# Kernel tuning notes

Measured on AMD Instinct MI355X. Metric: run time of the kernel, lower is better.

The kernel has to match this reference:

```python
import jax, jax.numpy as jnp
import numpy as np

DIM = 1024
HEADS = 16
HEAD_DIM = DIM // HEADS
RANK = 4
AUDIO_DIM = 768


def _lora(x, A, B):
    # x: [..., in]; A: [rank, in]; B: [out, rank]
    return x + (x @ A.T @ B.T) * (1.0 / RANK)


def setup_inputs() -> dict:
    key = jax.random.key(0)
    ks = jax.random.split(key, 20)
    s = 0.02
    inp = {
        "x": jax.random.normal(ks[0], (1, 4096, DIM), jnp.float32),
        "audio_features": jax.random.normal(ks[1], (1, 1024, AUDIO_DIM), jnp.float32),
        "q_w": jax.random.normal(ks[2], (DIM, DIM), jnp.float32) * s,
        "q_b": jnp.zeros((DIM,), jnp.float32),
        "k_w": jax.random.normal(ks[3], (DIM, DIM), jnp.float32) * s,
        "k_b": jnp.zeros((DIM,), jnp.float32),
        "v_w": jax.random.normal(ks[4], (DIM, DIM), jnp.float32) * s,
        "v_b": jnp.zeros((DIM,), jnp.float32),
        "o_w": jax.random.normal(ks[5], (DIM, DIM), jnp.float32) * s,
        "o_b": jnp.zeros((DIM,), jnp.float32),
        "a_w": jax.random.normal(ks[6], (DIM, AUDIO_DIM), jnp.float32) * s,
        "a_b": jnp.zeros((DIM,), jnp.float32),
        "qA": jax.random.normal(ks[7], (RANK, DIM), jnp.float32) * 0.01,
        "qB": jax.random.normal(ks[8], (DIM, RANK), jnp.float32) * 0.01,
        "kA": jax.random.normal(ks[9], (RANK, DIM), jnp.float32) * 0.01,
        "kB": jax.random.normal(ks[10], (DIM, RANK), jnp.float32) * 0.01,
        "vA": jax.random.normal(ks[11], (RANK, DIM), jnp.float32) * 0.01,
        "vB": jax.random.normal(ks[12], (DIM, RANK), jnp.float32) * 0.01,
    }
    return inp


def reference(x, audio_features, q_w, q_b, k_w, k_b, v_w, v_b, o_w, o_b,
              a_w, a_b, qA, qB, kA, kB, vA, vB):
    B, N, C = x.shape
    # audio projection: Linear(768 -> dim), torch Linear is x @ W.T + b
    audio = audio_features @ a_w.T + a_b  # [B, M, C]
    M = audio.shape[1]

    q = _lora(x @ q_w.T + q_b, qA, qB)      # [B, N, C]
    k = _lora(audio @ k_w.T + k_b, kA, kB)  # [B, M, C]
    v = _lora(audio @ v_w.T + v_b, vA, vB)  # [B, M, C]

    q = q.reshape(B, N, HEADS, HEAD_DIM).transpose(0, 2, 1, 3)  # [B,H,N,d]
    k = k.reshape(B, M, HEADS, HEAD_DIM).transpose(0, 2, 1, 3)  # [B,H,M,d]
    v = v.reshape(B, M, HEADS, HEAD_DIM).transpose(0, 2, 1, 3)  # [B,H,M,d]

    scale = HEAD_DIM ** -0.5
    attn = jnp.einsum('bhnd,bhmd->bhnm', q, k) * scale  # [B,H,N,M]
    attn = jax.nn.softmax(attn, axis=-1)
    out = jnp.einsum('bhnm,bhmd->bhnd', attn, v)        # [B,H,N,d]
    out = out.transpose(0, 2, 1, 3).reshape(B, N, C)
    return out @ o_w.T + o_b
```

## Files before the change

kernel.cpp:

```cpp
#include <hip/hip_runtime.h>
#include <math.h>

#define DIM 1024
#define HEADS 16
#define HD 64
#define QSCALE 0.1803368801111204f

typedef __attribute__((ext_vector_type(8))) short short8;
typedef __attribute__((ext_vector_type(4))) float f32x4;
typedef unsigned short ushort_t;

#define MFMA(a, b, c) __builtin_amdgcn_mfma_f32_16x16x32_bf16(a, b, c, 0, 0, 0)
#define VMCNT(n) asm volatile("s_waitcnt vmcnt(" #n ")" ::: "memory")
#define BARRIER() __builtin_amdgcn_s_barrier()

__device__ __forceinline__ ushort_t f2bf(float f) {
    union { float f; unsigned u; } v; v.f = f;
    unsigned r = v.u + 0x7FFF + ((v.u >> 16) & 1);
    return (ushort_t)(r >> 16);
}
__device__ __forceinline__ void gl2lds16(const void* g, void* l) {
    __builtin_amdgcn_global_load_lds(
        (const __attribute__((address_space(1))) unsigned*)g,
        (__attribute__((address_space(3))) unsigned*)l, 16, 0, 0);
}

#define C_X  1048576
#define C_AF 196608
__global__ __launch_bounds__(256) void prep1(
    const float* __restrict__ x, const float* __restrict__ af,
    const float* __restrict__ aw, const float* __restrict__ ow,
    ushort_t* __restrict__ xb, ushort_t* __restrict__ afb,
    ushort_t* __restrict__ awb, ushort_t* __restrict__ owb,
    const float* __restrict__ qw, const float* __restrict__ kw,
    const float* __restrict__ vw,
    const float* __restrict__ qA, const float* __restrict__ kA,
    const float* __restrict__ vA,
    float* __restrict__ part)
{
    const int b = blockIdx.x, tid = threadIdx.x;
    if (b >= 48) {
        int c = (b - 48) * 256 + tid;
        const float* s; ushort_t* d; int off;
        if (c < C_X)               { s = x;  d = xb;  off = c; }
        else if (c < C_X + C_AF)   { s = af; d = afb; off = c - C_X; }
        else if (c < C_X + 2*C_AF) { s = aw; d = awb; off = c - C_X - C_AF; }
        else                       { s = ow; d = owb; off = c - C_X - 2*C_AF; }
        float4 v = ((const float4*)s)[off];
        ushort4 o = { f2bf(v.x), f2bf(v.y), f2bf(v.z), f2bf(v.w) };
        ((ushort4*)d)[off] = o;
        return;
    }
    const int pb = b;
    const int proj = pb >> 4, chunk = pb & 15;
    const float* W = proj == 0 ? qw : proj == 1 ? kw : vw;
    const float* A = proj == 0 ? qA : proj == 1 ? kA : vA;
    const float4* W4 = (const float4*)W;

    float4 acc0 = {0,0,0,0}, acc1 = {0,0,0,0}, acc2 = {0,0,0,0}, acc3 = {0,0,0,0};
    const int o0 = chunk * 64;
    for (int o = o0; o < o0 + 64; ++o) {
        float4 wrow = W4[o * 256 + tid];
        float a0 = A[o], a1 = A[1024 + o], a2 = A[2048 + o], a3 = A[3072 + o];
        acc0.x += a0 * wrow.x; acc0.y += a0 * wrow.y; acc0.z += a0 * wrow.z; acc0.w += a0 * wrow.w;
        acc1.x += a1 * wrow.x; acc1.y += a1 * wrow.y; acc1.z += a1 * wrow.z; acc1.w += a1 * wrow.w;
        acc2.x += a2 * wrow.x; acc2.y += a2 * wrow.y; acc2.z += a2 * wrow.z; acc2.w += a2 * wrow.w;
        acc3.x += a3 * wrow.x; acc3.y += a3 * wrow.y; acc3.z += a3 * wrow.z; acc3.w += a3 * wrow.w;
    }
    float4* P4 = (float4*)part;
    P4[(pb * 4 + 0) * 256 + tid] = acc0;
    P4[(pb * 4 + 1) * 256 + tid] = acc1;
    P4[(pb * 4 + 2) * 256 + tid] = acc2;
    P4[(pb * 4 + 3) * 256 + tid] = acc3;
}

__global__ __launch_bounds__(256) void prep2(
    const float* __restrict__ qw, const float* __restrict__ kw,
    const float* __restrict__ vw,
    const float* __restrict__ qA, const float* __restrict__ kA,
    const float* __restrict__ vA,
    const float* __restrict__ qB, const float* __restrict__ kB,
    const float* __restrict__ vB,
    const float* __restrict__ qb, const float* __restrict__ kb,
    const float* __restrict__ vb,
    const float* __restrict__ part,
    ushort_t* __restrict__ wqe, ushort_t* __restrict__ wke,
    ushort_t* __restrict__ wve, float* __restrict__ beff)
{
    const int b = blockIdx.x, tid = threadIdx.x;
    const int proj = b >> 4, chunk = b & 15;
    const float* W = proj == 0 ? qw : proj == 1 ? kw : vw;
    const float* A = proj == 0 ? qA : proj == 1 ? kA : vA;
    const float* B = proj == 0 ? qB : proj == 1 ? kB : vB;
    const float* bias = proj == 0 ? qb : proj == 1 ? kb : vb;
    ushort_t* Weff = proj == 0 ? wqe : proj == 1 ? wke : wve;
    const float scale = proj == 0 ? QSCALE : 1.0f;
    const float4* W4 = (const float4*)W;
    const float4* P4 = (const float4*)part;

    __shared__ float T1s[4096];
    #pragma unroll
    for (int r = 0; r < 4; ++r) {
        float4 s = {0, 0, 0, 0};
        for (int blk = 0; blk < 16; ++blk) {
            float4 p = P4[((proj * 16 + blk) * 4 + r) * 256 + tid];
            s.x += p.x; s.y += p.y; s.z += p.z; s.w += p.w;
        }
        *(float4*)(T1s + r * 1024 + tid * 4) = s;
    }
    __syncthreads();

    float4 t0 = *(const float4*)(T1s + tid * 4);
    float4 t1 = *(const float4*)(T1s + 1024 + tid * 4);
    float4 t2 = *(const float4*)(T1s + 2048 + tid * 4);
    float4 t3 = *(const float4*)(T1s + 3072 + tid * 4);

    const int o0 = chunk * 64;
    for (int o = o0; o < o0 + 64; ++o) {
        float4 wrow = W4[o * 256 + tid];
        float4 Bo = *(const float4*)(B + o * 4);
        ushort4 out;
        out.x = f2bf((wrow.x + 0.25f * (Bo.x*t0.x + Bo.y*t1.x + Bo.z*t2.x + Bo.w*t3.x)) * scale);
        out.y = f2bf((wrow.y + 0.25f * (Bo.x*t0.y + Bo.y*t1.y + Bo.z*t2.y + Bo.w*t3.y)) * scale);
        out.z = f2bf((wrow.z + 0.25f * (Bo.x*t0.z + Bo.y*t1.z + Bo.z*t2.z + Bo.w*t3.z)) * scale);
        out.w = f2bf((wrow.w + 0.25f * (Bo.x*t0.w + Bo.y*t1.w + Bo.z*t2.w + Bo.w*t3.w)) * scale);
        *(ushort4*)(Weff + (size_t)o * 1024 + tid * 4) = out;
    }

    if (chunk == 0) {
        float bt[4] = {0.f, 0.f, 0.f, 0.f};
        for (int o = tid; o < 1024; o += 256) {
            float bo = bias[o];
            bt[0] = fmaf(A[o], bo, bt[0]);
            bt[1] = fmaf(A[1024 + o], bo, bt[1]);
            bt[2] = fmaf(A[2048 + o], bo, bt[2]);
            bt[3] = fmaf(A[3072 + o], bo, bt[3]);
        }
        #pragma unroll
        for (int r = 0; r < 4; ++r)
            #pragma unroll
            for (int off = 32; off; off >>= 1) bt[r] += __shfl_xor(bt[r], off);
        __shared__ float btr[4][4];
        if ((tid & 63) == 0) {
            #pragma unroll
            for (int r = 0; r < 4; ++r) btr[r][tid >> 6] = bt[r];
        }
        __syncthreads();
        float b0 = btr[0][0] + btr[0][1] + btr[0][2] + btr[0][3];
        float b1 = btr[1][0] + btr[1][1] + btr[1][2] + btr[1][3];
        float b2 = btr[2][0] + btr[2][1] + btr[2][2] + btr[2][3];
        float b3 = btr[3][0] + btr[3][1] + btr[3][2] + btr[3][3];
        for (int o = tid; o < 1024; o += 256) {
            float4 Bo = *(const float4*)(B + o * 4);
            beff[proj * 1024 + o] =
                (bias[o] + 0.25f * (Bo.x*b0 + Bo.y*b1 + Bo.z*b2 + Bo.w*b3)) * scale;
        }
    }
}

template<int OUTF32>
__device__ __forceinline__ void gemm4_body(
    char* lds, const ushort_t* __restrict__ A, const ushort_t* __restrict__ W,
    const float* __restrict__ bias, void* __restrict__ C,
    int N, int K, int bm, int bn)
{
    const int tid = threadIdx.x, lane = tid & 63, wv = tid >> 6;
    const int l15 = lane & 15, l4 = lane >> 4;
    const int wm = wv >> 1, wn = wv & 1;

    const ushort_t *Ag[2], *Wg;
    #pragma unroll
    for (int c = 0; c < 2; ++c) {
        int f = c * 256 + tid, ra = f >> 2, ga = (f & 3) ^ ((ra >> 1) & 3);
        Ag[c] = A + (size_t)(bm * 128 + ra) * K + ga * 8;
    }
    {
        int f = tid, rb = f >> 2, gb = (f & 3) ^ ((rb >> 1) & 3);
        Wg = W + (size_t)(bn * 64 + rb) * K + gb * 8;
    }
    int aoff[4], woff[2];
    #pragma unroll
    for (int m = 0; m < 4; ++m) {
        int r = wm * 64 + m * 16 + l15;
        aoff[m] = r * 64 + ((l4 ^ ((r >> 1) & 3)) << 4);
    }
    #pragma unroll
    for (int n = 0; n < 2; ++n) {
        int cc = wn * 32 + n * 16 + l15;
        woff[n] = cc * 64 + ((l4 ^ ((cc >> 1) & 3)) << 4);
    }

    auto stage = [&](char* base, int k0) {
        gl2lds16(Ag[0] + k0, base + wv * 1024);
        gl2lds16(Ag[1] + k0, base + 4096 + wv * 1024);
        gl2lds16(Wg + k0, base + 8192 + wv * 1024);
    };

    short8 fa[4], fw[2];
    auto readfr = [&](const char* base) {
        #pragma unroll
        for (int m = 0; m < 4; ++m) fa[m] = *(const short8*)(base + aoff[m]);
        #pragma unroll
        for (int n = 0; n < 2; ++n) fw[n] = *(const short8*)(base + 8192 + woff[n]);
    };

    f32x4 acc[4][2] = {};
    const int nt = K / 32;

    stage(lds, 0);
    stage(lds + 12288, 32);
    VMCNT(3);
    BARRIER();
    readfr(lds);

    int bcur = 0;
    for (int t = 0; t < nt; ++t) {
        int bnext = bcur + 1; if (bnext == 3) bnext = 0;
        int bpre  = bnext + 1; if (bpre == 3) bpre = 0;
        if (t + 2 < nt) stage(lds + bpre * 12288, (t + 2) * 32);
        #pragma unroll
        for (int m = 0; m < 4; ++m)
            #pragma unroll
            for (int n = 0; n < 2; ++n)
                acc[m][n] = MFMA(fa[m], fw[n], acc[m][n]);
        if (t + 1 < nt) {
            if (t + 2 < nt) { VMCNT(3); } else { VMCNT(0); }
            BARRIER();
            readfr(lds + bnext * 12288);
        }
        bcur = bnext;
    }

    #pragma unroll
    for (int n = 0; n < 2; ++n) {
        int gc = bn * 64 + wn * 32 + n * 16 + l15;
        float bv = bias[gc];
        #pragma unroll
        for (int m = 0; m < 4; ++m) {
            int gr = bm * 128 + wm * 64 + m * 16 + (l4 << 2);
            #pragma unroll
            for (int j = 0; j < 4; ++j) {
                float v = acc[m][n][j] + bv;
                if (OUTF32) ((float*)C)[(size_t)(gr + j) * N + gc] = v;
                else        ((ushort_t*)C)[(size_t)(gr + j) * N + gc] = f2bf(v);
            }
        }
    }
}

template<int OUTF32>
__global__ __launch_bounds__(256) void gemm4(
    const ushort_t* __restrict__ A, const ushort_t* __restrict__ W,
    const float* __restrict__ bias, void* __restrict__ C, int N, int K)
{
    __shared__ char lds[36864];
    gemm4_body<OUTF32>(lds, A, W, bias, C, N, K, blockIdx.y, blockIdx.x);
}

__device__ __forceinline__ void audio_body(
    char* lds, const ushort_t* __restrict__ A, const ushort_t* __restrict__ W,
    const float* __restrict__ bias, ushort_t* __restrict__ C, int bm, int bn)
{
    const int K = 768, N = DIM;
    char* As = lds;
    char* Ws = lds + 8192;
    const int tid = threadIdx.x, lane = tid & 63, wv = tid >> 6;
    const int l15 = lane & 15, l4 = lane >> 4;

    int f = tid, ra = f >> 2, ga = (f & 3) ^ ((ra >> 1) & 3);
    const ushort_t* Ag = A + (size_t)(bm * 64 + ra) * K + ga * 8;
    const ushort_t* Wg = W + (size_t)(bn * 64 + ra) * K + ga * 8;

    int aoff, woff[4];
    { int r = wv * 16 + l15; aoff = r * 64 + ((l4 ^ ((r >> 1) & 3)) << 4); }
    #pragma unroll
    for (int n = 0; n < 4; ++n) {
        int cc = n * 16 + l15;
        woff[n] = cc * 64 + ((l4 ^ ((cc >> 1) & 3)) << 4);
    }

    f32x4 acc[4] = {};
    const int nt = K / 32;
    gl2lds16(Ag, As + wv * 1024);
    gl2lds16(Wg, Ws + wv * 1024);

    for (int t = 0; t < nt; ++t) {
        const int buf = t & 1;
        if (t + 1 < nt) {
            const int k1 = (t + 1) * 32;
            gl2lds16(Ag + k1, As + (buf ^ 1) * 4096 + wv * 1024);
            gl2lds16(Wg + k1, Ws + (buf ^ 1) * 4096 + wv * 1024);
            VMCNT(2);
        } else {
            VMCNT(0);
        }
        BARRIER();
        const char* AsB = As + buf * 4096;
        const char* WsB = Ws + buf * 4096;
        short8 fa = *(const short8*)(AsB + aoff);
        short8 fw[4];
        #pragma unroll
        for (int n = 0; n < 4; ++n) fw[n] = *(const short8*)(WsB + woff[n]);
        #pragma unroll
        for (int n = 0; n < 4; ++n) acc[n] = MFMA(fa, fw[n], acc[n]);
        BARRIER();
    }

    const int gr = bm * 64 + wv * 16 + (l4 << 2);
    #pragma unroll
    for (int n = 0; n < 4; ++n) {
        int gc = bn * 64 + n * 16 + l15;
        float bb = bias[gc];
        #pragma unroll
        for (int j = 0; j < 4; ++j)
            C[(size_t)(gr + j) * N + gc] = f2bf(acc[n][j] + bb);
    }
}

__global__ __launch_bounds__(256) void fused_aq(
    const ushort_t* __restrict__ afb, const ushort_t* __restrict__ awb,
    const float* __restrict__ a_b, ushort_t* __restrict__ audio,
    const ushort_t* __restrict__ xb, const ushort_t* __restrict__ wqe,
    const float* __restrict__ beff, ushort_t* __restrict__ qbb)
{
    __shared__ char lds[36864];
    const int b = blockIdx.x;
    if (b < 256) {
        audio_body(lds, afb, awb, a_b, audio, b >> 4, b & 15);
    } else {
        const int i = b - 256;
        gemm4_body<0>(lds, xb, wqe, beff, qbb, DIM, DIM, i >> 4, i & 15);
    }
}

__global__ __launch_bounds__(256) void gemm2_kv(
    const ushort_t* __restrict__ A, const ushort_t* __restrict__ Wk,
    const ushort_t* __restrict__ Wv, const float* __restrict__ bk,
    const float* __restrict__ bv, ushort_t* __restrict__ Ck,
    ushort_t* __restrict__ CvT)
{
    const int K = DIM;
    __shared__ ushort_t As[2][64 * 32];
    __shared__ ushort_t Ws[2][64 * 32];
    const int tid = threadIdx.x, lane = tid & 63, wv = tid >> 6;
    const int l15 = lane & 15, l4 = lane >> 4;
    const int bm = blockIdx.y;
    const bool isV = blockIdx.x >= 16;
    const int bn = blockIdx.x & 15;
    const ushort_t* W = isV ? Wv : Wk;

    int f = tid, ra = f >> 2, ga = (f & 3) ^ ((ra >> 1) & 3);
    const ushort_t* Ag = A + (size_t)(bm * 64 + ra) * K + ga * 8;
    const ushort_t* Wg = W + (size_t)(bn * 64 + ra) * K + ga * 8;

    int aoff, woff[4];
    { int r = wv * 16 + l15; aoff = r * 64 + ((l4 ^ ((r >> 1) & 3)) << 4); }
    #pragma unroll
    for (int n = 0; n < 4; ++n) {
        int cc = n * 16 + l15;
        woff[n] = cc * 64 + ((l4 ^ ((cc >> 1) & 3)) << 4);
    }

    f32x4 acc[4] = {};
    const int nt = K / 32;
    gl2lds16(Ag, (char*)As + wv * 1024);
    gl2lds16(Wg, (char*)Ws + wv * 1024);

    for (int t = 0; t < nt; ++t) {
        const int buf = t & 1;
        if (t + 1 < nt) {
            const int k1 = (t + 1) * 32;
            gl2lds16(Ag + k1, (char*)As + (buf ^ 1) * 4096 + wv * 1024);
            gl2lds16(Wg + k1, (char*)Ws + (buf ^ 1) * 4096 + wv * 1024);
            VMCNT(2);
        } else {
            VMCNT(0);
        }
        BARRIER();
        const char* AsB = (const char*)As + buf * 4096;
        const char* WsB = (const char*)Ws + buf * 4096;
        short8 fa = *(const short8*)(AsB + aoff);
        short8 fw[4];
        #pragma unroll
        for (int n = 0; n < 4; ++n) fw[n] = *(const short8*)(WsB + woff[n]);
        #pragma unroll
        for (int n = 0; n < 4; ++n) acc[n] = MFMA(fa, fw[n], acc[n]);
        BARRIER();
    }

    const int gr = bm * 64 + wv * 16 + (l4 << 2);
    #pragma unroll
    for (int n = 0; n < 4; ++n) {
        int gc = bn * 64 + n * 16 + l15;
        float bb = (isV ? bv : bk)[gc];
        if (!isV) {
            #pragma unroll
            for (int j = 0; j < 4; ++j)
                Ck[(size_t)(gr + j) * DIM + gc] = f2bf(acc[n][j] + bb);
        } else {
            ushort4 o = { f2bf(acc[n][0] + bb), f2bf(acc[n][1] + bb),
                          f2bf(acc[n][2] + bb), f2bf(acc[n][3] + bb) };
            *(ushort4*)(CvT + (size_t)gc * DIM + gr) = o;
        }
    }
}

__global__ __launch_bounds__(256) void attn3(
    const ushort_t* __restrict__ Qf, const ushort_t* __restrict__ Kf,
    const ushort_t* __restrict__ Vt, ushort_t* __restrict__ AO)
{
    __shared__ char lds[40960];
    char* QsPs = lds;
    char* KsB0 = lds + 8192;
    char* VsB0 = lds + 24576;

    const int tid = threadIdx.x, lane = tid & 63, wv = tid >> 6;
    const int l15 = lane & 15, l4 = lane >> 4;
    const int h = blockIdx.y, qb = blockIdx.x;

    #pragma unroll
    for (int i = 0; i < 2; ++i) {
        int f = i * 256 + tid, q = f >> 3, s = (f & 7) ^ (q & 7);
        gl2lds16(Qf + (size_t)(qb * 64 + q) * DIM + h * HD + s * 8,
                 QsPs + i * 4096 + wv * 1024);
    }
    const int f0 = tid, r0 = f0 >> 3, s0 = (f0 & 7) ^ (r0 & 7);
    const int f1 = 256 + tid, r1 = f1 >> 3, s1 = (f1 & 7) ^ (r1 & 7);
    const ushort_t* Kg0 = Kf + (size_t)r0 * DIM + h * HD + s0 * 8;
    const ushort_t* Kg1 = Kf + (size_t)r1 * DIM + h * HD + s1 * 8;
    const ushort_t* Vg0 = Vt + (size_t)(h * HD + r0) * DIM + s0 * 8;
    const ushort_t* Vg1 = Vt + (size_t)(h * HD + r1) * DIM + s1 * 8;

    int qoff[2], koff[4][2], poff[2];
    #pragma unroll
    for (int ks = 0; ks < 2; ++ks) {
        int r = wv * 16 + l15;
        qoff[ks] = r * 128 + (((ks * 4 + l4) ^ (r & 7)) << 4);
        poff[ks] = wv * 2048 + l15 * 128 + (((ks * 4 + l4) ^ (l15 & 7)) << 4);
    }
    #pragma unroll
    for (int n = 0; n < 4; ++n) {
        int kk = n * 16 + l15;
        #pragma unroll
        for (int ks = 0; ks < 2; ++ks)
            koff[n][ks] = kk * 128 + (((ks * 4 + l4) ^ (kk & 7)) << 4);
    }

    f32x4 acc_o[4] = {};
    float l_loc[4] = {0.f, 0.f, 0.f, 0.f};

    gl2lds16(Kg0, KsB0 + wv * 1024);
    gl2lds16(Kg1, KsB0 + 4096 + wv * 1024);
    gl2lds16(Vg0, VsB0 + wv * 1024);
    gl2lds16(Vg1, VsB0 + 4096 + wv * 1024);
    VMCNT(4);
    BARRIER();
    short8 fq[2];
    #pragma unroll
    for (int ks = 0; ks < 2; ++ks)
        fq[ks] = *(const short8*)(QsPs + qoff[ks]);

    for (int t = 0; t < 16; ++t) {
        const int buf = t & 1;
        if (t < 15) {
            gl2lds16(Kg0 + (size_t)(t + 1) * 64 * DIM,
                     KsB0 + (buf ^ 1) * 8192 + wv * 1024);
            gl2lds16(Kg1 + (size_t)(t + 1) * 64 * DIM,
                     KsB0 + (buf ^ 1) * 8192 + 4096 + wv * 1024);
            gl2lds16(Vg0 + (t + 1) * 64,
                     VsB0 + (buf ^ 1) * 8192 + wv * 1024);
            gl2lds16(Vg1 + (t + 1) * 64,
                     VsB0 + (buf ^ 1) * 8192 + 4096 + wv * 1024);
            VMCNT(4);
        } else {
            VMCNT(0);
        }
        BARRIER();

        const char* KsT = KsB0 + buf * 8192;
        const char* VsT = VsB0 + buf * 8192;

        f32x4 s_acc[4] = {};
        short8 fk[4][2];
        #pragma unroll
        for (int n = 0; n < 4; ++n)
            #pragma unroll
            for (int ks = 0; ks < 2; ++ks)
                fk[n][ks] = *(const short8*)(KsT + koff[n][ks]);
        #pragma unroll
        for (int n = 0; n < 4; ++n)
            #pragma unroll
            for (int ks = 0; ks < 2; ++ks)
                s_acc[n] = MFMA(fq[ks], fk[n][ks], s_acc[n]);

        #pragma unroll
        for (int j = 0; j < 4; ++j) {
            float p0 = exp2f(s_acc[0][j]);
            float p1 = exp2f(s_acc[1][j]);
            float p2 = exp2f(s_acc[2][j]);
            float p3 = exp2f(s_acc[3][j]);
            l_loc[j] += (p0 + p1) + (p2 + p3);
            unsigned pk01, pk23;
            asm("v_cvt_pk_bf16_f32 %0, %1, %2" : "=v"(pk01) : "v"(p0), "v"(p1));
            asm("v_cvt_pk_bf16_f32 %0, %1, %2" : "=v"(pk23) : "v"(p2), "v"(p3));
            int r16 = (l4 << 2) + j;
            int basb = wv * 2048 + r16 * 128;
            int sw = (r16 & 7) << 4;
            int kx = l15 * 2;
            *(ushort_t*)(QsPs + basb + ((kx) ^ sw))      = (ushort_t)pk01;
            *(ushort_t*)(QsPs + basb + ((32 + kx) ^ sw)) = (ushort_t)(pk01 >> 16);
            *(ushort_t*)(QsPs + basb + ((64 + kx) ^ sw)) = (ushort_t)pk23;
            *(ushort_t*)(QsPs + basb + ((96 + kx) ^ sw)) = (ushort_t)(pk23 >> 16);
        }

        short8 pa[2], fv[4][2];
        #pragma unroll
        for (int ks = 0; ks < 2; ++ks)
            pa[ks] = *(const short8*)(QsPs + poff[ks]);
        #pragma unroll
        for (int n = 0; n < 4; ++n)
            #pragma unroll
            for (int ks = 0; ks < 2; ++ks)
                fv[n][ks] = *(const short8*)(VsT + koff[n][ks]);
        #pragma unroll
        for (int dn = 0; dn < 4; ++dn)
            #pragma unroll
            for (int ks = 0; ks < 2; ++ks)
                acc_o[dn] = MFMA(pa[ks], fv[dn][ks], acc_o[dn]);
        BARRIER();
    }

    #pragma unroll
    for (int j = 0; j < 4; ++j) {
        float l = l_loc[j];
        l += __shfl_xor(l, 1);
        l += __shfl_xor(l, 2);
        l += __shfl_xor(l, 4);
        l += __shfl_xor(l, 8);
        float inv = 1.0f / l;
        int q = qb * 64 + wv * 16 + (l4 << 2) + j;
        #pragma unroll
        for (int dn = 0; dn < 4; ++dn)
            AO[(size_t)q * DIM + h * HD + dn * 16 + l15] =
                f2bf(acc_o[dn][j] * inv);
    }
}

extern "C" void kernel_launch(void* const* d_in, const int* in_sizes, int n_in,
                              void* d_out, int out_size, void* d_ws, size_t ws_size,
                              hipStream_t stream)
{
    const float* x   = (const float*)d_in[0];
    const float* af  = (const float*)d_in[1];
    const float* q_w = (const float*)d_in[2];
    const float* q_b = (const float*)d_in[3];
    const float* k_w = (const float*)d_in[4];
    const float* k_b = (const float*)d_in[5];
    const float* v_w = (const float*)d_in[6];
    const float* v_b = (const float*)d_in[7];
    const float* o_w = (const float*)d_in[8];
    const float* o_b = (const float*)d_in[9];
    const float* a_w = (const float*)d_in[10];
    const float* a_b = (const float*)d_in[11];
    const float* qA  = (const float*)d_in[12];
    const float* qB  = (const float*)d_in[13];
    const float* kA  = (const float*)d_in[14];
    const float* kB  = (const float*)d_in[15];
    const float* vA  = (const float*)d_in[16];
    const float* vB  = (const float*)d_in[17];
    float* out = (float*)d_out;

    const int N = 4096;

    char* w = (char*)d_ws;
    auto alloc = [&](size_t bytes) {
        char* p = w; w += (bytes + 255) & ~(size_t)255; return p;
    };
    ushort_t* xb   = (ushort_t*)alloc((size_t)N * DIM * 2);
    ushort_t* afb  = (ushort_t*)alloc((size_t)1024 * 768 * 2);
    ushort_t* awb  = (ushort_t*)alloc((size_t)DIM * 768 * 2);
    ushort_t* owb  = (ushort_t*)alloc((size_t)DIM * DIM * 2);
    ushort_t* wqe  = (ushort_t*)alloc((size_t)DIM * DIM * 2);
    ushort_t* wke  = (ushort_t*)alloc((size_t)DIM * DIM * 2);
    ushort_t* wve  = (ushort_t*)alloc((size_t)DIM * DIM * 2);
    ushort_t* audio= (ushort_t*)alloc((size_t)1024 * DIM * 2);
    ushort_t* qbb  = (ushort_t*)alloc((size_t)N * DIM * 2);
    ushort_t* kbb  = (ushort_t*)alloc((size_t)1024 * DIM * 2);
    ushort_t* vt   = (ushort_t*)alloc((size_t)1024 * DIM * 2);
    ushort_t* ao   = (ushort_t*)alloc((size_t)N * DIM * 2);
    float* part = (float*)alloc((size_t)48 * 4 * 1024 * 4);
    float* beff = (float*)alloc((size_t)3 * 1024 * 4);

    prep1<<<6704, 256, 0, stream>>>(
        x, af, a_w, o_w, xb, afb, awb, owb,
        q_w, k_w, v_w, qA, kA, vA, part);
    prep2<<<48, 256, 0, stream>>>(
        q_w, k_w, v_w, qA, kA, vA, qB, kB, vB, q_b, k_b, v_b,
        part, wqe, wke, wve, beff);
    fused_aq<<<768, 256, 0, stream>>>(afb, awb, a_b, audio, xb, wqe, beff, qbb);
    gemm2_kv<<<dim3(32, 16), 256, 0, stream>>>(audio, wke, wve,
                                               beff + 1024, beff + 2048, kbb, vt);
    attn3<<<dim3(N / 64, HEADS), 256, 0, stream>>>(qbb, kbb, vt, ao);
    gemm4<1><<<dim3(16, 32), 256, 0, stream>>>(ao, owb, o_b, out, DIM, DIM);
}
```

Baseline: 229.7 us.

## Double query rows per attention block and grid-stride the conversion kernel

```diff
diff --git a/kernel.cpp b/kernel.cpp
--- a/kernel.cpp
+++ b/kernel.cpp
@@ -27,6 +27,8 @@
 
 #define C_X  1048576
 #define C_AF 196608
+#define C_OW 262144
+#define TOT4 (C_X + 2 * C_AF + C_OW)
 __global__ __launch_bounds__(256) void prep1(
     const float* __restrict__ x, const float* __restrict__ af,
     const float* __restrict__ aw, const float* __restrict__ ow,
@@ -40,15 +42,16 @@
 {
     const int b = blockIdx.x, tid = threadIdx.x;
     if (b >= 48) {
-        int c = (b - 48) * 256 + tid;
-        const float* s; ushort_t* d; int off;
-        if (c < C_X)               { s = x;  d = xb;  off = c; }
-        else if (c < C_X + C_AF)   { s = af; d = afb; off = c - C_X; }
-        else if (c < C_X + 2*C_AF) { s = aw; d = awb; off = c - C_X - C_AF; }
-        else                       { s = ow; d = owb; off = c - C_X - 2*C_AF; }
-        float4 v = ((const float4*)s)[off];
-        ushort4 o = { f2bf(v.x), f2bf(v.y), f2bf(v.z), f2bf(v.w) };
-        ((ushort4*)d)[off] = o;
+        for (int c = (b - 48) * 256 + tid; c < TOT4; c += 2048 * 256) {
+            const float* s; ushort_t* d; int off;
+            if (c < C_X)               { s = x;  d = xb;  off = c; }
+            else if (c < C_X + C_AF)   { s = af; d = afb; off = c - C_X; }
+            else if (c < C_X + 2*C_AF) { s = aw; d = awb; off = c - C_X - C_AF; }
+            else                       { s = ow; d = owb; off = c - C_X - 2*C_AF; }
+            float4 v = ((const float4*)s)[off];
+            ushort4 o = { f2bf(v.x), f2bf(v.y), f2bf(v.z), f2bf(v.w) };
+            ((ushort4*)d)[off] = o;
+        }
         return;
     }
     const int pb = b;
@@ -405,23 +408,23 @@
     }
 }
 
-__global__ __launch_bounds__(256) void attn3(
+__global__ __launch_bounds__(256) void attn5(
     const ushort_t* __restrict__ Qf, const ushort_t* __restrict__ Kf,
     const ushort_t* __restrict__ Vt, ushort_t* __restrict__ AO)
 {
-    __shared__ char lds[40960];
+    __shared__ char lds[49152];
     char* QsPs = lds;
-    char* KsB0 = lds + 8192;
-    char* VsB0 = lds + 24576;
+    char* KsB0 = lds + 16384;
+    char* VsB0 = lds + 32768;
 
     const int tid = threadIdx.x, lane = tid & 63, wv = tid >> 6;
     const int l15 = lane & 15, l4 = lane >> 4;
     const int h = blockIdx.y, qb = blockIdx.x;
 
     #pragma unroll
-    for (int i = 0; i < 2; ++i) {
+    for (int i = 0; i < 4; ++i) {
         int f = i * 256 + tid, q = f >> 3, s = (f & 7) ^ (q & 7);
-        gl2lds16(Qf + (size_t)(qb * 64 + q) * DIM + h * HD + s * 8,
+        gl2lds16(Qf + (size_t)(qb * 128 + q) * DIM + h * HD + s * 8,
                  QsPs + i * 4096 + wv * 1024);
     }
     const int f0 = tid, r0 = f0 >> 3, s0 = (f0 & 7) ^ (r0 & 7);
@@ -431,13 +434,16 @@
     const ushort_t* Vg0 = Vt + (size_t)(h * HD + r0) * DIM + s0 * 8;
     const ushort_t* Vg1 = Vt + (size_t)(h * HD + r1) * DIM + s1 * 8;
 
-    int qoff[2], koff[4][2], poff[2];
-    #pragma unroll
-    for (int ks = 0; ks < 2; ++ks) {
-        int r = wv * 16 + l15;
-        qoff[ks] = r * 128 + (((ks * 4 + l4) ^ (r & 7)) << 4);
-        poff[ks] = wv * 2048 + l15 * 128 + (((ks * 4 + l4) ^ (l15 & 7)) << 4);
-    }
+    int qoff[2][2], poff[2][2], koff[4][2];
+    #pragma unroll
+    for (int m = 0; m < 2; ++m)
+        #pragma unroll
+        for (int ks = 0; ks < 2; ++ks) {
+            int r = wv * 32 + m * 16 + l15;
+            qoff[m][ks] = r * 128 + (((ks * 4 + l4) ^ (r & 7)) << 4);
+            int rp = m * 16 + l15;
+            poff[m][ks] = wv * 4096 + rp * 128 + (((ks * 4 + l4) ^ (rp & 7)) << 4);
+        }
     #pragma unroll
     for (int n = 0; n < 4; ++n) {
         int kk = n * 16 + l15;
@@ -446,8 +452,8 @@
             koff[n][ks] = kk * 128 + (((ks * 4 + l4) ^ (kk & 7)) << 4);
     }
 
-    f32x4 acc_o[4] = {};
-    float l_loc[4] = {0.f, 0.f, 0.f, 0.f};
+    f32x4 acc_o[2][4] = {};
+    float l_loc[2][4] = {};
 
     gl2lds16(Kg0, KsB0 + wv * 1024);
     gl2lds16(Kg1, KsB0 + 4096 + wv * 1024);
@@ -455,10 +461,12 @@
     gl2lds16(Vg1, VsB0 + 4096 + wv * 1024);
     VMCNT(4);
     BARRIER();
-    short8 fq[2];
-    #pragma unroll
-    for (int ks = 0; ks < 2; ++ks)
-        fq[ks] = *(const short8*)(QsPs + qoff[ks]);
+    short8 fq[2][2];
+    #pragma unroll
+    for (int m = 0; m < 2; ++m)
+        #pragma unroll
+        for (int ks = 0; ks < 2; ++ks)
+            fq[m][ks] = *(const short8*)(QsPs + qoff[m][ks]);
 
     for (int t = 0; t < 16; ++t) {
         const int buf = t & 1;
@@ -480,70 +488,80 @@
         const char* KsT = KsB0 + buf * 8192;
         const char* VsT = VsB0 + buf * 8192;
 
-        f32x4 s_acc[4] = {};
         short8 fk[4][2];
         #pragma unroll
         for (int n = 0; n < 4; ++n)
             #pragma unroll
             for (int ks = 0; ks < 2; ++ks)
                 fk[n][ks] = *(const short8*)(KsT + koff[n][ks]);
-        #pragma unroll
-        for (int n = 0; n < 4; ++n)
+        f32x4 s_acc[2][4] = {};
+        #pragma unroll
+        for (int m = 0; m < 2; ++m)
+            #pragma unroll
+            for (int n = 0; n < 4; ++n)
+                #pragma unroll
+                for (int ks = 0; ks < 2; ++ks)
+                    s_acc[m][n] = MFMA(fq[m][ks], fk[n][ks], s_acc[m][n]);
+
+        #pragma unroll
+        for (int m = 0; m < 2; ++m)
+            #pragma unroll
+            for (int j = 0; j < 4; ++j) {
+                float p0 = exp2f(s_acc[m][0][j]);
+                float p1 = exp2f(s_acc[m][1][j]);
+                float p2 = exp2f(s_acc[m][2][j]);
+                float p3 = exp2f(s_acc[m][3][j]);
+                l_loc[m][j] += (p0 + p1) + (p2 + p3);
+                unsigned pk01, pk23;
+                asm("v_cvt_pk_bf16_f32 %0, %1, %2" : "=v"(pk01) : "v"(p0), "v"(p1));
+                asm("v_cvt_pk_bf16_f32 %0, %1, %2" : "=v"(pk23) : "v"(p2), "v"(p3));
+                int r32 = m * 16 + (l4 << 2) + j;
+                int basb = wv * 4096 + r32 * 128;
+                int sw = (r32 & 7) << 4;
+                int kx = l15 * 2;
+                *(ushort_t*)(QsPs + basb + ((kx) ^ sw))      = (ushort_t)pk01;
+                *(ushort_t*)(QsPs + basb + ((32 + kx) ^ sw)) = (ushort_t)(pk01 >> 16);
+                *(ushort_t*)(QsPs + basb + ((64 + kx) ^ sw)) = (ushort_t)pk23;
+                *(ushort_t*)(QsPs + basb + ((96 + kx) ^ sw)) = (ushort_t)(pk23 >> 16);
+            }
+
+        short8 pa[2][2], fv[4][2];
+        #pragma unroll
+        for (int m = 0; m < 2; ++m)
             #pragma unroll
             for (int ks = 0; ks < 2; ++ks)
-                s_acc[n] = MFMA(fq[ks], fk[n][ks], s_acc[n]);
-
-        #pragma unroll
-        for (int j = 0; j < 4; ++j) {
-            float p0 = exp2f(s_acc[0][j]);
-            float p1 = exp2f(s_acc[1][j]);
-            float p2 = exp2f(s_acc[2][j]);
-            float p3 = exp2f(s_acc[3][j]);
-            l_loc[j] += (p0 + p1) + (p2 + p3);
-            unsigned pk01, pk23;
-            asm("v_cvt_pk_bf16_f32 %0, %1, %2" : "=v"(pk01) : "v"(p0), "v"(p1));
-            asm("v_cvt_pk_bf16_f32 %0, %1, %2" : "=v"(pk23) : "v"(p2), "v"(p3));
-            int r16 = (l4 << 2) + j;
-            int basb = wv * 2048 + r16 * 128;
-            int sw = (r16 & 7) << 4;
-            int kx = l15 * 2;
-            *(ushort_t*)(QsPs + basb + ((kx) ^ sw))      = (ushort_t)pk01;
-            *(ushort_t*)(QsPs + basb + ((32 + kx) ^ sw)) = (ushort_t)(pk01 >> 16);
-            *(ushort_t*)(QsPs + basb + ((64 + kx) ^ sw)) = (ushort_t)pk23;
-            *(ushort_t*)(QsPs + basb + ((96 + kx) ^ sw)) = (ushort_t)(pk23 >> 16);
-        }
-
-        short8 pa[2], fv[4][2];
-        #pragma unroll
-        for (int ks = 0; ks < 2; ++ks)
-            pa[ks] = *(const short8*)(QsPs + poff[ks]);
+                pa[m][ks] = *(const short8*)(QsPs + poff[m][ks]);
         #pragma unroll
         for (int n = 0; n < 4; ++n)
             #pragma unroll
             for (int ks = 0; ks < 2; ++ks)
                 fv[n][ks] = *(const short8*)(VsT + koff[n][ks]);
         #pragma unroll
-        for (int dn = 0; dn < 4; ++dn)
-            #pragma unroll
-            for (int ks = 0; ks < 2; ++ks)
-                acc_o[dn] = MFMA(pa[ks], fv[dn][ks], acc_o[dn]);
+        for (int m = 0; m < 2; ++m)
+            #pragma unroll
+            for (int dn = 0; dn < 4; ++dn)
+                #pragma unroll
+                for (int ks = 0; ks < 2; ++ks)
+                    acc_o[m][dn] = MFMA(pa[m][ks], fv[dn][ks], acc_o[m][dn]);
         BARRIER();
     }
 
     #pragma unroll
-    for (int j = 0; j < 4; ++j) {
-        float l = l_loc[j];
-        l += __shfl_xor(l, 1);
-        l += __shfl_xor(l, 2);
-        l += __shfl_xor(l, 4);
-        l += __shfl_xor(l, 8);
-        float inv = 1.0f / l;
-        int q = qb * 64 + wv * 16 + (l4 << 2) + j;
-        #pragma unroll
-        for (int dn = 0; dn < 4; ++dn)
-            AO[(size_t)q * DIM + h * HD + dn * 16 + l15] =
-                f2bf(acc_o[dn][j] * inv);
-    }
+    for (int m = 0; m < 2; ++m)
+        #pragma unroll
+        for (int j = 0; j < 4; ++j) {
+            float l = l_loc[m][j];
+            l += __shfl_xor(l, 1);
+            l += __shfl_xor(l, 2);
+            l += __shfl_xor(l, 4);
+            l += __shfl_xor(l, 8);
+            float inv = 1.0f / l;
+            int q = qb * 128 + wv * 32 + m * 16 + (l4 << 2) + j;
+            #pragma unroll
+            for (int dn = 0; dn < 4; ++dn)
+                AO[(size_t)q * DIM + h * HD + dn * 16 + l15] =
+                    f2bf(acc_o[m][dn][j] * inv);
+        }
 }
 
 extern "C" void kernel_launch(void* const* d_in, const int* in_sizes, int n_in,
@@ -591,7 +609,7 @@
     float* part = (float*)alloc((size_t)48 * 4 * 1024 * 4);
     float* beff = (float*)alloc((size_t)3 * 1024 * 4);
 
-    prep1<<<6704, 256, 0, stream>>>(
+    prep1<<<2096, 256, 0, stream>>>(
         x, af, a_w, o_w, xb, afb, awb, owb,
         q_w, k_w, v_w, qA, kA, vA, part);
     prep2<<<48, 256, 0, stream>>>(
@@ -600,6 +618,6 @@
     fused_aq<<<768, 256, 0, stream>>>(afb, awb, a_b, audio, xb, wqe, beff, qbb);
     gemm2_kv<<<dim3(32, 16), 256, 0, stream>>>(audio, wke, wve,
                                                beff + 1024, beff + 2048, kbb, vt);
-    attn3<<<dim3(N / 64, HEADS), 256, 0, stream>>>(qbb, kbb, vt, ao);
+    attn5<<<dim3(N / 128, HEADS), 256, 0, stream>>>(qbb, kbb, vt, ao);
     gemm4<1><<<dim3(16, 32), 256, 0, stream>>>(ao, owb, o_b, out, DIM, DIM);
 }
```

Measured after the change: 232.1 us. No clear change (+1.0%).
